# Kernel optimization log

Hardware: AMD Instinct MI355X
Metric: run time of the kernel (lower is better)

## Reference

```python
import jax, jax.numpy as jnp
import numpy as np

# dims
B, S, A = 16384, 300, 30
EMB, M_TOK, M_PROTO = 256, 8, 16
H_ENC, H_DEC, MF, NZ = 256, 128, 12, 4
ALPHA_MIN, ALPHA_MAX, ETA0 = 0.06, 0.3, 0.1
TECH_IDX = jnp.array([61, 91, 121, 151, 181, 211, 241, 271])


def setup_inputs() -> dict:
    key = jax.random.key(0)
    ks = jax.random.split(key, 20)
    def w(k, shape, fan):
        return jax.random.normal(k, shape, jnp.float32) * (fan ** -0.5)
    return {
        'state':   jax.random.uniform(ks[0], (B, S), jnp.float32),
        'fitness': jax.random.uniform(ks[1], (B, M_PROTO), jnp.float32),
        'proto_keys': jax.random.normal(ks[2], (M_PROTO, EMB), jnp.float32) * (EMB ** -0.5),
        'enc_W1': w(ks[3], (S, H_ENC), S),   'enc_b1': jnp.zeros((H_ENC,), jnp.float32),
        'ln_g':   jnp.ones((H_ENC,), jnp.float32), 'ln_b': jnp.zeros((H_ENC,), jnp.float32),
        'enc_W2': w(ks[4], (H_ENC, M_TOK * EMB), H_ENC), 'enc_b2': jnp.zeros((M_TOK * EMB,), jnp.float32),
        'dec_W1': w(ks[5], (M_PROTO, EMB, H_DEC), EMB),  'dec_b1': jnp.zeros((M_PROTO, H_DEC), jnp.float32),
        'dec_W2': w(ks[6], (M_PROTO, H_DEC, A), H_DEC),  'dec_b2': jnp.zeros((M_PROTO, A), jnp.float32),
        'tc_W':  w(ks[7], (MF, EMB), MF),  'tc_b':  jnp.zeros((EMB,), jnp.float32),
        'tc_cW': w(ks[8], (EMB, 1), EMB),  'tc_cb': jnp.zeros((1,), jnp.float32),
        'tc_zW': w(ks[9], (EMB, NZ), EMB), 'tc_zb': jnp.zeros((NZ,), jnp.float32),
        'w_prev': jnp.full((1, M_PROTO), 1.0 / M_PROTO, jnp.float32),
    }


def _layernorm(x, g, b, eps=1e-5):
    mu = x.mean(-1, keepdims=True)
    var = ((x - mu) ** 2).mean(-1, keepdims=True)
    return (x - mu) * jax.lax.rsqrt(var + eps) * g + b


def _forward(state, fitness, proto_keys, enc_W1, enc_b1, ln_g, ln_b, enc_W2, enc_b2,
             dec_W1, dec_b1, dec_W2, dec_b2, tc_W, tc_b, tc_cW, tc_cb, tc_zW, tc_zb, w_prev):
    # --- market feature extraction ---
    balance = state[:, 0:1]
    prices = state[:, 1:31]
    shares = state[:, 31:61]
    price_mean = prices.mean(1, keepdims=True)
    price_std = jnp.std(prices, axis=1, keepdims=True, ddof=1) + 1e-8  # torch.std is unbiased
    total_value = balance + (prices * shares).sum(1, keepdims=True)
    cash_ratio = balance / (total_value + 1e-8)
    tech = state[:, TECH_IDX]
    mf = jnp.concatenate([balance, price_mean, price_std, cash_ratio, tech], axis=1)  # [B,12]
    # --- T-Cell (minimal surrogate: danger embed, crisis level, crisis types) ---
    danger = jnp.tanh(mf @ tc_W + tc_b)                     # [B,EMB]
    crisis = jax.nn.sigmoid(danger @ tc_cW + tc_cb)         # [B,1]
    z = jax.nn.softmax(danger @ tc_zW + tc_zb, axis=-1)     # [B,NZ]
    # --- epitope encoder: Linear -> LN -> ReLU -> Linear -> reshape [B,m,EMB] ---
    h = jax.nn.relu(_layernorm(state @ enc_W1 + enc_b1, ln_g, ln_b))
    E = (h @ enc_W2 + enc_b2).reshape(-1, M_TOK, EMB)
    # --- IRT routing (OT-attention + fitness replicator, crisis-gated mix) ---
    scale = EMB ** -0.5
    logits = jnp.einsum('bme,ne->bmn', E, proto_keys) * scale \
           + (jnp.einsum('be,ne->bn', danger, proto_keys) * scale)[:, None, :]  # [B,m,M]
    P = jax.nn.softmax(logits, axis=-1)
    w_ot = P.mean(axis=1)                                   # [B,M]
    w_rep = w_prev * jnp.exp(ETA0 * fitness)
    w_rep = w_rep / (w_rep.sum(-1, keepdims=True) + 1e-8)
    alpha_c = ALPHA_MIN + (ALPHA_MAX - ALPHA_MIN) * (1.0 - crisis)  # [B,1]
    w = alpha_c * w_ot + (1.0 - alpha_c) * w_rep
    w = w / (w.sum(-1, keepdims=True) + 1e-8)
    # --- per-expert decoders on proto_keys (batched GEMM over M experts) ---
    hd = jax.nn.relu(jnp.einsum('me,meh->mh', proto_keys, dec_W1) + dec_b1)
    conc = jax.nn.softplus(jnp.einsum('mh,mha->ma', hd, dec_W2) + dec_b2)  # [M,A]
    mixed = jnp.einsum('bm,ma->ba', w, conc) + 1.0          # [B,A]
    # deterministic branch: softmax action head
    action = jax.nn.softmax(mixed, axis=-1)
    action = jnp.clip(action, 0.0, 1.0)
    action = action / (action.sum(-1, keepdims=True) + 1e-8)
    return action


def reference(state, fitness, proto_keys, enc_W1, enc_b1, ln_g, ln_b, enc_W2, enc_b2,
              dec_W1, dec_b1, dec_W2, dec_b2, tc_W, tc_b, tc_cW, tc_cb, tc_zW, tc_zb, w_prev):
    return _forward(state, fitness, proto_keys, enc_W1, enc_b1, ln_g, ln_b, enc_W2, enc_b2,
                    dec_W1, dec_b1, dec_W2, dec_b2, tc_W, tc_b, tc_cW, tc_cb, tc_zW, tc_zb, w_prev)
```

## Files before the change

kernel.cpp:

```cpp
#include <hip/hip_runtime.h>

typedef __attribute__((ext_vector_type(8))) short bf16x8;
typedef __attribute__((ext_vector_type(4))) float f32x4;

#define NBATCH 16384
#define SS     300
#define AA     30
#define ROWS   32
#define SSTR   352
#define HSTR   280
#define LSTR   132
#define K1P    320
#define SCALEF 0.0625f
#define ETA0   0.1f

__device__ __forceinline__ short f2b(float x) {
    unsigned u = __float_as_uint(x);
    unsigned r = (u + 0x7FFFu + ((u >> 16) & 1u)) >> 16;
    return (short)r;
}
__device__ __forceinline__ float b2f(short s) {
    return __uint_as_float(((unsigned)(unsigned short)s) << 16);
}
__device__ __forceinline__ float tanh_fast(float x) {
    float e = __expf(2.f * x);
    return 1.f - 2.f / (e + 1.f);
}

__global__ __launch_bounds__(256) void pre_kernel(
    const float* __restrict__ proto, const float* __restrict__ W2,
    const float* __restrict__ b2,   const float* __restrict__ W1,
    const float* __restrict__ dW1,  const float* __restrict__ db1,
    const float* __restrict__ dW2,  const float* __restrict__ db2,
    short* __restrict__ W1T, short* __restrict__ W3T, short* __restrict__ protoB,
    float* __restrict__ cmn, float* __restrict__ conc)
{
    const int t = threadIdx.x;
    const int bid = blockIdx.x;
    if (bid < 128) {
        const int c = bid, m = c >> 4, n = c & 15;
        __shared__ float pr[256];
        pr[t] = proto[n * 256 + t];
        __syncthreads();
        const float* w2 = W2 + (size_t)t * 2048 + m * 256;
        float acc = 0.f;
        #pragma unroll 8
        for (int e = 0; e < 256; ++e) acc += w2[e] * pr[e];
        W3T[c * 256 + t] = f2b(acc);
        if (t == 0) {
            float ca = 0.f;
            for (int e = 0; e < 256; ++e) ca += b2[m * 256 + e] * pr[e];
            cmn[c] = ca;
        }
    } else if (bid < 144) {
        const int m = bid - 128;
        __shared__ float hd[128];
        if (t < 128) {
            float acc = db1[m * 128 + t];
            const float* w = dW1 + (size_t)m * 256 * 128 + t;
            const float* p = proto + m * 256;
            for (int e = 0; e < 256; ++e) acc += p[e] * w[e * 128];
            hd[t] = fmaxf(acc, 0.f);
        }
        __syncthreads();
        if (t < AA) {
            float acc = db2[m * AA + t];
            const float* w = dW2 + (size_t)m * 128 * AA + t;
            for (int h = 0; h < 128; ++h) acc += hd[h] * w[h * AA];
            conc[m * AA + t] = fmaxf(acc, 0.f) + log1pf(__expf(-fabsf(acc)));
        }
    } else if (bid < 160) {
        const int bn = bid - 144;
        const int nl = t >> 4, kl = t & 15;
        const int n = bn * 16 + nl;
        for (int it = 0; it < 20; ++it) {
            const int k = kl + it * 16;
            const float v = (k < SS) ? W1[(size_t)k * 256 + n] : 0.f;
            W1T[n * K1P + k] = f2b(v);
        }
    } else {
        for (int i = t; i < 16 * 256; i += 256) protoB[i] = f2b(proto[i]);
    }
}

__global__ __launch_bounds__(256, 3) void main_kernel(
    const float* __restrict__ state, const float* __restrict__ fitness,
    const float* __restrict__ b1,
    const float* __restrict__ ln_g, const float* __restrict__ ln_b,
    const float* __restrict__ tcW,  const float* __restrict__ tcb,
    const float* __restrict__ cW,   const float* __restrict__ cb,
    const float* __restrict__ pw,
    const short* __restrict__ W1T,  const short* __restrict__ W3T,
    const short* __restrict__ protoB,
    const float* __restrict__ cmn,  const float* __restrict__ conc,
    float* __restrict__ out)
{
    const int t    = threadIdx.x;
    const int row0 = blockIdx.x * ROWS;
    const int w    = t >> 6;
    const int lane = t & 63;
    const int l15  = lane & 15;
    const int q    = lane >> 4;

    __shared__ short sA[ROWS * SSTR];
    __shared__ short sB[ROWS * HSTR];
    __shared__ float s_mf[ROWS][12];
    __shared__ float s_red[ROWS][8];
    __shared__ float s_mu[ROWS], s_rstd[ROWS];
    __shared__ float s_ddot[ROWS * 16];
    __shared__ float s_crisis[ROWS];
    __shared__ float s_cmn[128];
    __shared__ float s_conc[16 * AA];

    float* s_log  = (float*)sB;
    float* s_wrep = (float*)&sA[ROWS * HSTR];

    for (int idx = t; idx < ROWS * K1P; idx += 256) {
        const int r = idx / K1P, k = idx - r * K1P;
        sA[r * SSTR + k] = (k < SS) ? f2b(state[(size_t)(row0 + r) * SS + k]) : (short)0;
    }
    for (int idx = t; idx < 128 + 16 * AA; idx += 256) {
        if (idx < 128) s_cmn[idx] = cmn[idx];
        else s_conc[idx - 128] = conc[idx - 128];
    }
    __syncthreads();

    {
        const int r = t >> 3, g = t & 7;
        float sp = 0.f, sp2 = 0.f, sps = 0.f;
        const int i0 = g * 4, i1 = (g == 7) ? 2 : 4;
        for (int i = 0; i < i1; ++i) {
            const float p = b2f(sA[r * SSTR + 1 + i0 + i]);
            const float s = b2f(sA[r * SSTR + 31 + i0 + i]);
            sp += p; sp2 += p * p; sps += p * s;
        }
        for (int off = 1; off < 8; off <<= 1) {
            sp  += __shfl_xor(sp, off);
            sp2 += __shfl_xor(sp2, off);
            sps += __shfl_xor(sps, off);
        }
        s_mf[r][4 + g] = b2f(sA[r * SSTR + 61 + 30 * g]);
        if (g == 0) {
            const float bal = b2f(sA[r * SSTR + 0]);
            const float pm = sp * (1.f / 30.f);
            const float var = (sp2 - 30.f * pm * pm) * (1.f / 29.f);
            const float pstd = sqrtf(fmaxf(var, 0.f)) + 1e-8f;
            const float tv = bal + sps;
            s_mf[r][0] = bal; s_mf[r][1] = pm; s_mf[r][2] = pstd;
            s_mf[r][3] = bal / (tv + 1e-8f);
        }
    }
    __syncthreads();

    {
        float wreg[12];
        #pragma unroll
        for (int k = 0; k < 12; ++k) wreg[k] = tcW[k * 256 + t];
        const float tb = tcb[t];
        for (int r = 0; r < ROWS; ++r) {
            float acc = tb;
            #pragma unroll
            for (int k = 0; k < 12; ++k) acc = fmaf(s_mf[r][k], wreg[k], acc);
            sB[r * HSTR + t] = f2b(tanh_fast(acc));
        }
    }
    __syncthreads();

    if (w < 2) {
        f32x4 accd = {0.f, 0.f, 0.f, 0.f};
        const int mt = w;
        for (int kt = 0; kt < 8; ++kt) {
            bf16x8 a = *(const bf16x8*)&sB[(mt * 16 + l15) * HSTR + kt * 32 + q * 8];
            bf16x8 b = *(const bf16x8*)&protoB[l15 * 256 + kt * 32 + q * 8];
            accd = __builtin_amdgcn_mfma_f32_16x16x32_bf16(a, b, accd, 0, 0, 0);
        }
        #pragma unroll
        for (int reg = 0; reg < 4; ++reg) {
            const int row = mt * 16 + q * 4 + reg;
            s_ddot[row * 16 + l15] = accd[reg];
        }
    } else {
        const float4 cw = *(const float4*)&cW[lane * 4];
        const float cbv = cb[0];
        for (int rr = 0; rr < 16; ++rr) {
            const int row = (w - 2) * 16 + rr;
            const short* dp = &sB[row * HSTR + lane * 4];
            float p = b2f(dp[0]) * cw.x + b2f(dp[1]) * cw.y
                    + b2f(dp[2]) * cw.z + b2f(dp[3]) * cw.w;
            for (int off = 32; off; off >>= 1) p += __shfl_down(p, off);
            if (lane == 0) s_crisis[row] = 1.f / (1.f + __expf(-(p + cbv)));
        }
    }

    f32x4 acc[2][4];
    #pragma unroll
    for (int mt = 0; mt < 2; ++mt)
        #pragma unroll
        for (int u = 0; u < 4; ++u) acc[mt][u] = (f32x4){0.f, 0.f, 0.f, 0.f};
    for (int kt = 0; kt < 10; ++kt) {
        bf16x8 a0 = *(const bf16x8*)&sA[l15 * SSTR + kt * 32 + q * 8];
        bf16x8 a1 = *(const bf16x8*)&sA[(l15 + 16) * SSTR + kt * 32 + q * 8];
        bf16x8 bfr[4];
        #pragma unroll
        for (int u = 0; u < 4; ++u)
            bfr[u] = *(const bf16x8*)&W1T[(w * 64 + u * 16 + l15) * K1P + kt * 32 + q * 8];
        #pragma unroll
        for (int u = 0; u < 4; ++u) {
            acc[0][u] = __builtin_amdgcn_mfma_f32_16x16x32_bf16(a0, bfr[u], acc[0][u], 0, 0, 0);
            acc[1][u] = __builtin_amdgcn_mfma_f32_16x16x32_bf16(a1, bfr[u], acc[1][u], 0, 0, 0);
        }
    }

    {
        float b1v[4];
        #pragma unroll
        for (int u = 0; u < 4; ++u) b1v[u] = b1[w * 64 + u * 16 + l15];
        #pragma unroll
        for (int mt = 0; mt < 2; ++mt) {
            #pragma unroll
            for (int reg = 0; reg < 4; ++reg) {
                float s = 0.f, s2 = 0.f;
                #pragma unroll
                for (int u = 0; u < 4; ++u) {
                    const float v = acc[mt][u][reg] + b1v[u];
                    acc[mt][u][reg] = v;
                    s += v; s2 += v * v;
                }
                for (int off = 1; off < 16; off <<= 1) {
                    s  += __shfl_xor(s, off);
                    s2 += __shfl_xor(s2, off);
                }
                if (l15 == 0) {
                    const int row = mt * 16 + q * 4 + reg;
                    s_red[row][w * 2]     = s;
                    s_red[row][w * 2 + 1] = s2;
                }
            }
        }
    }
    __syncthreads();
    if (t < ROWS) {
        float S = 0.f, S2 = 0.f;
        #pragma unroll
        for (int ww = 0; ww < 4; ++ww) { S += s_red[t][2 * ww]; S2 += s_red[t][2 * ww + 1]; }
        const float mu = S * (1.f / 256.f);
        const float var = S2 * (1.f / 256.f) - mu * mu;
        s_mu[t] = mu; s_rstd[t] = rsqrtf(var + 1e-5f);
    }
    __syncthreads();

    {
        float gv[4], bv[4];
        #pragma unroll
        for (int u = 0; u < 4; ++u) {
            gv[u] = ln_g[w * 64 + u * 16 + l15];
            bv[u] = ln_b[w * 64 + u * 16 + l15];
        }
        #pragma unroll
        for (int mt = 0; mt < 2; ++mt)
            #pragma unroll
            for (int reg = 0; reg < 4; ++reg) {
                const int row = mt * 16 + q * 4 + reg;
                const float mu = s_mu[row], rs = s_rstd[row];
                #pragma unroll
                for (int u = 0; u < 4; ++u) {
                    const int col = w * 64 + u * 16 + l15;
                    const float v = fmaxf((acc[mt][u][reg] - mu) * rs * gv[u] + bv[u], 0.f);
                    sA[row * HSTR + col] = f2b(v);
                }
            }
    }
    __syncthreads();

    {
        f32x4 acc2[2][2];
        #pragma unroll
        for (int mt = 0; mt < 2; ++mt)
            #pragma unroll
            for (int ct = 0; ct < 2; ++ct) acc2[mt][ct] = (f32x4){0.f, 0.f, 0.f, 0.f};
        for (int kt = 0; kt < 8; ++kt) {
            bf16x8 a0 = *(const bf16x8*)&sA[l15 * HSTR + kt * 32 + q * 8];
            bf16x8 a1 = *(const bf16x8*)&sA[(l15 + 16) * HSTR + kt * 32 + q * 8];
            bf16x8 b0 = *(const bf16x8*)&W3T[(w * 32 + l15) * 256 + kt * 32 + q * 8];
            bf16x8 b1f = *(const bf16x8*)&W3T[(w * 32 + 16 + l15) * 256 + kt * 32 + q * 8];
            acc2[0][0] = __builtin_amdgcn_mfma_f32_16x16x32_bf16(a0, b0, acc2[0][0], 0, 0, 0);
            acc2[0][1] = __builtin_amdgcn_mfma_f32_16x16x32_bf16(a0, b1f, acc2[0][1], 0, 0, 0);
            acc2[1][0] = __builtin_amdgcn_mfma_f32_16x16x32_bf16(a1, b0, acc2[1][0], 0, 0, 0);
            acc2[1][1] = __builtin_amdgcn_mfma_f32_16x16x32_bf16(a1, b1f, acc2[1][1], 0, 0, 0);
        }
        const float cm0 = s_cmn[w * 32 + l15], cm1 = s_cmn[w * 32 + 16 + l15];
        #pragma unroll
        for (int mt = 0; mt < 2; ++mt)
            #pragma unroll
            for (int reg = 0; reg < 4; ++reg) {
                const int row = mt * 16 + q * 4 + reg;
                const float dd = s_ddot[row * 16 + l15];
                s_log[row * LSTR + w * 32 + l15]      = SCALEF * (acc2[mt][0][reg] + cm0 + dd);
                s_log[row * LSTR + w * 32 + 16 + l15] = SCALEF * (acc2[mt][1][reg] + cm1 + dd);
            }
    }
    __syncthreads();

    {
        const int r = t >> 3, m = t & 7;
        float* lg = &s_log[r * LSTR + m * 16];
        float mx = lg[0];
        #pragma unroll
        for (int n = 1; n < 16; ++n) mx = fmaxf(mx, lg[n]);
        float sum = 0.f, p[16];
        #pragma unroll
        for (int n = 0; n < 16; ++n) { p[n] = __expf(lg[n] - mx); sum += p[n]; }
        const float inv = 1.f / sum;
        #pragma unroll
        for (int n = 0; n < 16; ++n) lg[n] = p[n] * inv;
    }
    __syncthreads();

    for (int it = 0; it < 2; ++it) {
        const int idx = t + it * 256;
        const int r = idx >> 4, n = idx & 15;
        float wot = 0.f;
        #pragma unroll
        for (int m = 0; m < 8; ++m) wot += s_log[r * LSTR + m * 16 + n];
        s_ddot[idx] = wot * 0.125f;
        s_wrep[idx] = pw[n] * __expf(ETA0 * fitness[(size_t)(row0 + r) * 16 + n]);
    }
    __syncthreads();

    if (t < ROWS) {
        float srep = 0.f;
        #pragma unroll
        for (int n = 0; n < 16; ++n) srep += s_wrep[t * 16 + n];
        const float irep = 1.f / (srep + 1e-8f);
        const float alpha = 0.06f + 0.24f * (1.f - s_crisis[t]);
        float wn[16], sw = 0.f;
        #pragma unroll
        for (int n = 0; n < 16; ++n) {
            wn[n] = alpha * s_ddot[t * 16 + n] + (1.f - alpha) * s_wrep[t * 16 + n] * irep;
            sw += wn[n];
        }
        const float isw = 1.f / (sw + 1e-8f);
        #pragma unroll
        for (int n = 0; n < 16; ++n) s_ddot[t * 16 + n] = wn[n] * isw;
    }
    __syncthreads();

    {
        const int r = w * 8 + (lane >> 3);
        const int a0 = lane & 7;
        float wreg[16];
        #pragma unroll
        for (int n = 0; n < 16; ++n) wreg[n] = s_ddot[r * 16 + n];
        float mix[4];
        #pragma unroll
        for (int j = 0; j < 4; ++j) {
            const int a = a0 + 8 * j;
            if (a < AA) {
                float m = 1.f;
                #pragma unroll
                for (int n = 0; n < 16; ++n) m = fmaf(wreg[n], s_conc[n * AA + a], m);
                mix[j] = m;
            } else mix[j] = -1e30f;
        }
        float mx = fmaxf(fmaxf(mix[0], mix[1]), fmaxf(mix[2], mix[3]));
        for (int off = 1; off < 8; off <<= 1) mx = fmaxf(mx, __shfl_xor(mx, off));
        float se = 0.f;
        #pragma unroll
        for (int j = 0; j < 4; ++j) {
            if (a0 + 8 * j < AA) { mix[j] = __expf(mix[j] - mx); se += mix[j]; }
        }
        for (int off = 1; off < 8; off <<= 1) se += __shfl_xor(se, off);
        const float inv = 1.f / se;
        #pragma unroll
        for (int j = 0; j < 4; ++j) {
            const int a = a0 + 8 * j;
            if (a < AA) out[(size_t)(row0 + r) * AA + a] = mix[j] * inv;
        }
    }
}

extern "C" void kernel_launch(void* const* d_in, const int* in_sizes, int n_in,
                              void* d_out, int out_size, void* d_ws, size_t ws_size,
                              hipStream_t stream) {
    const float* state   = (const float*)d_in[0];
    const float* fitness = (const float*)d_in[1];
    const float* proto   = (const float*)d_in[2];
    const float* enc_W1  = (const float*)d_in[3];
    const float* enc_b1  = (const float*)d_in[4];
    const float* ln_g    = (const float*)d_in[5];
    const float* ln_b    = (const float*)d_in[6];
    const float* enc_W2  = (const float*)d_in[7];
    const float* enc_b2  = (const float*)d_in[8];
    const float* dec_W1  = (const float*)d_in[9];
    const float* dec_b1  = (const float*)d_in[10];
    const float* dec_W2  = (const float*)d_in[11];
    const float* dec_b2  = (const float*)d_in[12];
    const float* tc_W    = (const float*)d_in[13];
    const float* tc_b    = (const float*)d_in[14];
    const float* tc_cW   = (const float*)d_in[15];
    const float* tc_cb   = (const float*)d_in[16];
    const float* w_prev  = (const float*)d_in[19];
    float* out = (float*)d_out;

    short* W1T    = (short*)d_ws;
    short* W3T    = (short*)((char*)d_ws + 163840);
    short* protoB = (short*)((char*)d_ws + 229376);
    float* cmn    = (float*)((char*)d_ws + 237568);
    float* conc   = (float*)((char*)d_ws + 238080);

    pre_kernel<<<161, 256, 0, stream>>>(proto, enc_W2, enc_b2, enc_W1,
                                        dec_W1, dec_b1, dec_W2, dec_b2,
                                        W1T, W3T, protoB, cmn, conc);
    main_kernel<<<NBATCH / ROWS, 256, 0, stream>>>(state, fitness,
                                                   enc_b1, ln_g, ln_b,
                                                   tc_W, tc_b, tc_cW, tc_cb, w_prev,
                                                   W1T, W3T, protoB, cmn, conc, out);
}
```

Baseline: 155.0 us.

## Halve rows per block, pre-pack weights in MFMA fragment order, use MFMA for small GEMMs

Main kernel now handles 16 rows per block instead of 32, with launch bounds raised to 5 blocks per CU for higher occupancy. The pre-kernel repacks W1, W3, proto/crisis weights and tc_W into a layout that matches the MFMA B-fragment order, so each lane loads one contiguous 16-byte vector. The tech-feature projection and the crisis dot product now run as MFMA instead of scalar loops, and the W2·proto precompute also uses MFMA. The cost is that each block reuses weight loads across fewer rows, so global/L2 traffic for weights per output row goes up.

```diff
diff --git a/kernel.cpp b/kernel.cpp
--- a/kernel.cpp
+++ b/kernel.cpp
@@ -6,7 +6,7 @@
 #define NBATCH 16384
 #define SS     300
 #define AA     30
-#define ROWS   32
+#define ROWS   16
 #define SSTR   352
 #define HSTR   280
 #define LSTR   132
@@ -28,70 +28,121 @@
 }
 
 __global__ __launch_bounds__(256) void pre_kernel(
-    const float* __restrict__ proto, const float* __restrict__ W2,
-    const float* __restrict__ b2,   const float* __restrict__ W1,
+    const float* __restrict__ proto, const float* __restrict__ W1,
+    const float* __restrict__ W2,   const float* __restrict__ b2,
+    const float* __restrict__ tcW,  const float* __restrict__ cW,
     const float* __restrict__ dW1,  const float* __restrict__ db1,
     const float* __restrict__ dW2,  const float* __restrict__ db2,
-    short* __restrict__ W1T, short* __restrict__ W3T, short* __restrict__ protoB,
+    short* __restrict__ W1P, short* __restrict__ W3P,
+    short* __restrict__ PDP, short* __restrict__ TCP,
     float* __restrict__ cmn, float* __restrict__ conc)
 {
+    __shared__ short sbuf[64 * 264 + 4096];
     const int t = threadIdx.x;
     const int bid = blockIdx.x;
-    if (bid < 128) {
-        const int c = bid, m = c >> 4, n = c & 15;
-        __shared__ float pr[256];
-        pr[t] = proto[n * 256 + t];
+
+    if (bid < 32) {
+        const int m = bid >> 2, jt = bid & 3;
+        short* W2s = sbuf;
+        short* prS = sbuf + 64 * 264;
+        #pragma unroll 4
+        for (int it = 0; it < 64; ++it) {
+            const int idx = it * 256 + t, j = idx >> 8, e = idx & 255;
+            W2s[j * 264 + e] = f2b(W2[(size_t)(jt * 64 + j) * 2048 + m * 256 + e]);
+        }
+        for (int it = 0; it < 16; ++it) {
+            const int id = it * 256 + t, chunk = id >> 3, j8 = id & 7;
+            const int kt = chunk >> 6, rem = chunk & 63, q = rem >> 4, n = rem & 15;
+            prS[id] = f2b(proto[n * 256 + kt * 32 + q * 8 + j8]);
+        }
         __syncthreads();
-        const float* w2 = W2 + (size_t)t * 2048 + m * 256;
-        float acc = 0.f;
-        #pragma unroll 8
-        for (int e = 0; e < 256; ++e) acc += w2[e] * pr[e];
-        W3T[c * 256 + t] = f2b(acc);
-        if (t == 0) {
-            float ca = 0.f;
-            for (int e = 0; e < 256; ++e) ca += b2[m * 256 + e] * pr[e];
-            cmn[c] = ca;
-        }
-    } else if (bid < 144) {
-        const int m = bid - 128;
-        __shared__ float hd[128];
+        const int lane = t & 63, wv = t >> 6, l15 = lane & 15, q = lane >> 4;
+        f32x4 acc = {0.f, 0.f, 0.f, 0.f};
+        for (int kt = 0; kt < 8; ++kt) {
+            bf16x8 a = *(const bf16x8*)&W2s[(wv * 16 + l15) * 264 + kt * 32 + q * 8];
+            bf16x8 b = *(const bf16x8*)&prS[((kt * 4 + q) * 16 + l15) * 8];
+            acc = __builtin_amdgcn_mfma_f32_16x16x32_bf16(a, b, acc, 0, 0, 0);
+        }
+        #pragma unroll
+        for (int reg = 0; reg < 4; ++reg) {
+            const int jg = jt * 64 + wv * 16 + q * 4 + reg;
+            const int c = m * 16 + l15;
+            const int ktj = jg >> 5, qj = (jg >> 3) & 3, j8 = jg & 7;
+            W3P[((ktj * 4 + qj) * 128 + c) * 8 + j8] = f2b(acc[reg]);
+        }
+    } else if (bid < 42) {
+        const int kt = bid - 32;
+        short* W1s = sbuf;
+        #pragma unroll 4
+        for (int it = 0; it < 32; ++it) {
+            const int idx = it * 256 + t, k = idx >> 8, n = idx & 255;
+            const int kg = kt * 32 + k;
+            W1s[k * 256 + n] = (kg < SS) ? f2b(W1[(size_t)kg * 256 + n]) : (short)0;
+        }
+        __syncthreads();
+        for (int it = 0; it < 4; ++it) {
+            const int id = it * 256 + t, q = id >> 8, n = id & 255;
+            bf16x8 v;
+            #pragma unroll
+            for (int j = 0; j < 8; ++j) v[j] = W1s[(q * 8 + j) * 256 + n];
+            *(bf16x8*)&W1P[((kt * 4 + q) * 256 + n) * 8] = v;
+        }
+    } else if (bid == 42) {
+        for (int it = 0; it < 32; ++it) {
+            const int id = it * 256 + t, chunk = id >> 3, j8 = id & 7;
+            const int kt = chunk >> 7, q = (chunk >> 5) & 3, np = chunk & 31;
+            const int k = kt * 32 + q * 8 + j8;
+            float v = 0.f;
+            if (np < 16) v = proto[np * 256 + k];
+            else if (np == 16) v = cW[k];
+            PDP[id] = f2b(v);
+        }
+    } else if (bid == 43) {
+        for (int it = 0; it < 32; ++it) {
+            const int id = it * 256 + t, chunk = id >> 3, j8 = id & 7;
+            const int q = chunk >> 8, n = chunk & 255, k = q * 8 + j8;
+            TCP[id] = (k < 12) ? f2b(tcW[k * 256 + n]) : (short)0;
+        }
+    } else if (bid == 44) {
+        float* b2s = (float*)sbuf;
+        float* prF = (float*)sbuf + 2048;
+        for (int it = 0; it < 8; ++it)  b2s[it * 256 + t] = b2[it * 256 + t];
+        for (int it = 0; it < 16; ++it) prF[it * 256 + t] = proto[it * 256 + t];
+        __syncthreads();
+        if (t < 128) {
+            const int mq = t >> 4, n = t & 15;
+            float acc = 0.f;
+            for (int e = 0; e < 256; ++e) acc += b2s[mq * 256 + e] * prF[n * 256 + e];
+            cmn[t] = acc;
+        }
+    } else {
+        const int m = bid - 45;
+        float* hd = (float*)sbuf;
         if (t < 128) {
             float acc = db1[m * 128 + t];
-            const float* w = dW1 + (size_t)m * 256 * 128 + t;
+            const float* wp = dW1 + (size_t)m * 256 * 128 + t;
             const float* p = proto + m * 256;
-            for (int e = 0; e < 256; ++e) acc += p[e] * w[e * 128];
+            for (int e = 0; e < 256; ++e) acc += p[e] * wp[e * 128];
             hd[t] = fmaxf(acc, 0.f);
         }
         __syncthreads();
         if (t < AA) {
             float acc = db2[m * AA + t];
-            const float* w = dW2 + (size_t)m * 128 * AA + t;
-            for (int h = 0; h < 128; ++h) acc += hd[h] * w[h * AA];
+            const float* wp = dW2 + (size_t)m * 128 * AA + t;
+            for (int h = 0; h < 128; ++h) acc += hd[h] * wp[h * AA];
             conc[m * AA + t] = fmaxf(acc, 0.f) + log1pf(__expf(-fabsf(acc)));
         }
-    } else if (bid < 160) {
-        const int bn = bid - 144;
-        const int nl = t >> 4, kl = t & 15;
-        const int n = bn * 16 + nl;
-        for (int it = 0; it < 20; ++it) {
-            const int k = kl + it * 16;
-            const float v = (k < SS) ? W1[(size_t)k * 256 + n] : 0.f;
-            W1T[n * K1P + k] = f2b(v);
-        }
-    } else {
-        for (int i = t; i < 16 * 256; i += 256) protoB[i] = f2b(proto[i]);
-    }
-}
-
-__global__ __launch_bounds__(256, 3) void main_kernel(
+    }
+}
+
+__global__ __launch_bounds__(256, 5) void main_kernel(
     const float* __restrict__ state, const float* __restrict__ fitness,
     const float* __restrict__ b1,
-    const float* __restrict__ ln_g, const float* __restrict__ ln_b,
-    const float* __restrict__ tcW,  const float* __restrict__ tcb,
-    const float* __restrict__ cW,   const float* __restrict__ cb,
+    const float* __restrict__ lng,  const float* __restrict__ lnb,
+    const float* __restrict__ tcb,  const float* __restrict__ cb,
     const float* __restrict__ pw,
-    const short* __restrict__ W1T,  const short* __restrict__ W3T,
-    const short* __restrict__ protoB,
+    const short* __restrict__ W1P,  const short* __restrict__ W3P,
+    const short* __restrict__ PDP,  const short* __restrict__ TCP,
     const float* __restrict__ cmn,  const float* __restrict__ conc,
     float* __restrict__ out)
 {
@@ -104,10 +155,10 @@
 
     __shared__ short sA[ROWS * SSTR];
     __shared__ short sB[ROWS * HSTR];
-    __shared__ float s_mf[ROWS][12];
+    __shared__ short s_mfB[ROWS * 32];
     __shared__ float s_red[ROWS][8];
     __shared__ float s_mu[ROWS], s_rstd[ROWS];
-    __shared__ float s_ddot[ROWS * 16];
+    __shared__ float s_dd[ROWS * 16];
     __shared__ float s_crisis[ROWS];
     __shared__ float s_cmn[128];
     __shared__ float s_conc[16 * AA];
@@ -115,126 +166,132 @@
     float* s_log  = (float*)sB;
     float* s_wrep = (float*)&sA[ROWS * HSTR];
 
-    for (int idx = t; idx < ROWS * K1P; idx += 256) {
-        const int r = idx / K1P, k = idx - r * K1P;
+    #pragma unroll 4
+    for (int it = 0; it < 20; ++it) {
+        const int idx = it * 256 + t, r = idx / K1P, k = idx - r * K1P;
         sA[r * SSTR + k] = (k < SS) ? f2b(state[(size_t)(row0 + r) * SS + k]) : (short)0;
     }
-    for (int idx = t; idx < 128 + 16 * AA; idx += 256) {
-        if (idx < 128) s_cmn[idx] = cmn[idx];
-        else s_conc[idx - 128] = conc[idx - 128];
-    }
-    __syncthreads();
-
-    {
-        const int r = t >> 3, g = t & 7;
+    for (int it = t; it < 128 + 16 * AA; it += 256) {
+        if (it < 128) s_cmn[it] = cmn[it];
+        else s_conc[it - 128] = conc[it - 128];
+    }
+    __syncthreads();
+
+    {
+        const int r = t >> 4, g = t & 15;
         float sp = 0.f, sp2 = 0.f, sps = 0.f;
-        const int i0 = g * 4, i1 = (g == 7) ? 2 : 4;
-        for (int i = 0; i < i1; ++i) {
-            const float p = b2f(sA[r * SSTR + 1 + i0 + i]);
-            const float s = b2f(sA[r * SSTR + 31 + i0 + i]);
-            sp += p; sp2 += p * p; sps += p * s;
-        }
-        for (int off = 1; off < 8; off <<= 1) {
+        if (g < 15) {
+            #pragma unroll
+            for (int jj = 0; jj < 2; ++jj) {
+                const int i = 2 * g + jj;
+                const float p = b2f(sA[r * SSTR + 1 + i]);
+                const float s = b2f(sA[r * SSTR + 31 + i]);
+                sp += p; sp2 += p * p; sps += p * s;
+            }
+        }
+        #pragma unroll
+        for (int off = 1; off < 16; off <<= 1) {
             sp  += __shfl_xor(sp, off);
             sp2 += __shfl_xor(sp2, off);
             sps += __shfl_xor(sps, off);
         }
-        s_mf[r][4 + g] = b2f(sA[r * SSTR + 61 + 30 * g]);
+        if (g < 8) s_mfB[r * 32 + 4 + g] = sA[r * SSTR + 61 + 30 * g];
+        for (int k = 12 + g; k < 32; k += 16) s_mfB[r * 32 + k] = 0;
         if (g == 0) {
-            const float bal = b2f(sA[r * SSTR + 0]);
+            const float bal = b2f(sA[r * SSTR]);
             const float pm = sp * (1.f / 30.f);
             const float var = (sp2 - 30.f * pm * pm) * (1.f / 29.f);
             const float pstd = sqrtf(fmaxf(var, 0.f)) + 1e-8f;
-            const float tv = bal + sps;
-            s_mf[r][0] = bal; s_mf[r][1] = pm; s_mf[r][2] = pstd;
-            s_mf[r][3] = bal / (tv + 1e-8f);
-        }
-    }
-    __syncthreads();
-
-    {
-        float wreg[12];
-        #pragma unroll
-        for (int k = 0; k < 12; ++k) wreg[k] = tcW[k * 256 + t];
-        const float tb = tcb[t];
-        for (int r = 0; r < ROWS; ++r) {
-            float acc = tb;
-            #pragma unroll
-            for (int k = 0; k < 12; ++k) acc = fmaf(s_mf[r][k], wreg[k], acc);
-            sB[r * HSTR + t] = f2b(tanh_fast(acc));
-        }
-    }
-    __syncthreads();
-
-    if (w < 2) {
-        f32x4 accd = {0.f, 0.f, 0.f, 0.f};
-        const int mt = w;
+            s_mfB[r * 32 + 0] = sA[r * SSTR];
+            s_mfB[r * 32 + 1] = f2b(pm);
+            s_mfB[r * 32 + 2] = f2b(pstd);
+            s_mfB[r * 32 + 3] = f2b(bal / (bal + sps + 1e-8f));
+        }
+    }
+    __syncthreads();
+
+    {
+        f32x4 dacc[4];
+        #pragma unroll
+        for (int u = 0; u < 4; ++u) dacc[u] = (f32x4){0.f, 0.f, 0.f, 0.f};
+        bf16x8 a = *(const bf16x8*)&s_mfB[l15 * 32 + q * 8];
+        #pragma unroll
+        for (int u = 0; u < 4; ++u) {
+            bf16x8 b = *(const bf16x8*)&TCP[((q << 8) | (w * 64 + u * 16 + l15)) * 8];
+            dacc[u] = __builtin_amdgcn_mfma_f32_16x16x32_bf16(a, b, dacc[u], 0, 0, 0);
+        }
+        #pragma unroll
+        for (int u = 0; u < 4; ++u) {
+            const int col = w * 64 + u * 16 + l15;
+            const float tb = tcb[col];
+            #pragma unroll
+            for (int reg = 0; reg < 4; ++reg)
+                sB[(q * 4 + reg) * HSTR + col] = f2b(tanh_fast(dacc[u][reg] + tb));
+        }
+    }
+    __syncthreads();
+
+    if (w == 0) {
+        f32x4 acc = {0.f, 0.f, 0.f, 0.f};
         for (int kt = 0; kt < 8; ++kt) {
-            bf16x8 a = *(const bf16x8*)&sB[(mt * 16 + l15) * HSTR + kt * 32 + q * 8];
-            bf16x8 b = *(const bf16x8*)&protoB[l15 * 256 + kt * 32 + q * 8];
-            accd = __builtin_amdgcn_mfma_f32_16x16x32_bf16(a, b, accd, 0, 0, 0);
-        }
+            bf16x8 a = *(const bf16x8*)&sB[l15 * HSTR + kt * 32 + q * 8];
+            bf16x8 b = *(const bf16x8*)&PDP[((kt * 4 + q) * 32 + l15) * 8];
+            acc = __builtin_amdgcn_mfma_f32_16x16x32_bf16(a, b, acc, 0, 0, 0);
+        }
+        #pragma unroll
+        for (int reg = 0; reg < 4; ++reg)
+            s_dd[(q * 4 + reg) * 16 + l15] = acc[reg];
+    } else if (w == 1) {
+        f32x4 acc = {0.f, 0.f, 0.f, 0.f};
+        for (int kt = 0; kt < 8; ++kt) {
+            bf16x8 a = *(const bf16x8*)&sB[l15 * HSTR + kt * 32 + q * 8];
+            bf16x8 b = *(const bf16x8*)&PDP[((kt * 4 + q) * 32 + 16 + l15) * 8];
+            acc = __builtin_amdgcn_mfma_f32_16x16x32_bf16(a, b, acc, 0, 0, 0);
+        }
+        if (l15 == 0) {
+            const float cbv = cb[0];
+            #pragma unroll
+            for (int reg = 0; reg < 4; ++reg)
+                s_crisis[q * 4 + reg] = 1.f / (1.f + __expf(-(acc[reg] + cbv)));
+        }
+    }
+
+    f32x4 acc[4];
+    #pragma unroll
+    for (int u = 0; u < 4; ++u) acc[u] = (f32x4){0.f, 0.f, 0.f, 0.f};
+    for (int kt = 0; kt < 10; ++kt) {
+        bf16x8 a = *(const bf16x8*)&sA[l15 * SSTR + kt * 32 + q * 8];
+        bf16x8 bfr[4];
+        #pragma unroll
+        for (int u = 0; u < 4; ++u)
+            bfr[u] = *(const bf16x8*)&W1P[((kt * 4 + q) * 256 + (w * 64 + u * 16 + l15)) * 8];
+        #pragma unroll
+        for (int u = 0; u < 4; ++u)
+            acc[u] = __builtin_amdgcn_mfma_f32_16x16x32_bf16(a, bfr[u], acc[u], 0, 0, 0);
+    }
+
+    {
+        float b1v[4];
+        #pragma unroll
+        for (int u = 0; u < 4; ++u) b1v[u] = b1[w * 64 + u * 16 + l15];
         #pragma unroll
         for (int reg = 0; reg < 4; ++reg) {
-            const int row = mt * 16 + q * 4 + reg;
-            s_ddot[row * 16 + l15] = accd[reg];
-        }
-    } else {
-        const float4 cw = *(const float4*)&cW[lane * 4];
-        const float cbv = cb[0];
-        for (int rr = 0; rr < 16; ++rr) {
-            const int row = (w - 2) * 16 + rr;
-            const short* dp = &sB[row * HSTR + lane * 4];
-            float p = b2f(dp[0]) * cw.x + b2f(dp[1]) * cw.y
-                    + b2f(dp[2]) * cw.z + b2f(dp[3]) * cw.w;
-            for (int off = 32; off; off >>= 1) p += __shfl_down(p, off);
-            if (lane == 0) s_crisis[row] = 1.f / (1.f + __expf(-(p + cbv)));
-        }
-    }
-
-    f32x4 acc[2][4];
-    #pragma unroll
-    for (int mt = 0; mt < 2; ++mt)
-        #pragma unroll
-        for (int u = 0; u < 4; ++u) acc[mt][u] = (f32x4){0.f, 0.f, 0.f, 0.f};
-    for (int kt = 0; kt < 10; ++kt) {
-        bf16x8 a0 = *(const bf16x8*)&sA[l15 * SSTR + kt * 32 + q * 8];
-        bf16x8 a1 = *(const bf16x8*)&sA[(l15 + 16) * SSTR + kt * 32 + q * 8];
-        bf16x8 bfr[4];
-        #pragma unroll
-        for (int u = 0; u < 4; ++u)
-            bfr[u] = *(const bf16x8*)&W1T[(w * 64 + u * 16 + l15) * K1P + kt * 32 + q * 8];
-        #pragma unroll
-        for (int u = 0; u < 4; ++u) {
-            acc[0][u] = __builtin_amdgcn_mfma_f32_16x16x32_bf16(a0, bfr[u], acc[0][u], 0, 0, 0);
-            acc[1][u] = __builtin_amdgcn_mfma_f32_16x16x32_bf16(a1, bfr[u], acc[1][u], 0, 0, 0);
-        }
-    }
-
-    {
-        float b1v[4];
-        #pragma unroll
-        for (int u = 0; u < 4; ++u) b1v[u] = b1[w * 64 + u * 16 + l15];
-        #pragma unroll
-        for (int mt = 0; mt < 2; ++mt) {
-            #pragma unroll
-            for (int reg = 0; reg < 4; ++reg) {
-                float s = 0.f, s2 = 0.f;
-                #pragma unroll
-                for (int u = 0; u < 4; ++u) {
-                    const float v = acc[mt][u][reg] + b1v[u];
-                    acc[mt][u][reg] = v;
-                    s += v; s2 += v * v;
-                }
-                for (int off = 1; off < 16; off <<= 1) {
-                    s  += __shfl_xor(s, off);
-                    s2 += __shfl_xor(s2, off);
-                }
-                if (l15 == 0) {
-                    const int row = mt * 16 + q * 4 + reg;
-                    s_red[row][w * 2]     = s;
-                    s_red[row][w * 2 + 1] = s2;
-                }
+            float s = 0.f, s2 = 0.f;
+            #pragma unroll
+            for (int u = 0; u < 4; ++u) {
+                const float v = acc[u][reg] + b1v[u];
+                acc[u][reg] = v;
+                s += v; s2 += v * v;
+            }
+            #pragma unroll
+            for (int off = 1; off < 16; off <<= 1) {
+                s  += __shfl_xor(s, off);
+                s2 += __shfl_xor(s2, off);
+            }
+            if (l15 == 0) {
+                const int row = q * 4 + reg;
+                s_red[row][w * 2]     = s;
+                s_red[row][w * 2 + 1] = s2;
             }
         }
     }
@@ -253,55 +310,46 @@
         float gv[4], bv[4];
         #pragma unroll
         for (int u = 0; u < 4; ++u) {
-            gv[u] = ln_g[w * 64 + u * 16 + l15];
-            bv[u] = ln_b[w * 64 + u * 16 + l15];
-        }
-        #pragma unroll
-        for (int mt = 0; mt < 2; ++mt)
-            #pragma unroll
-            for (int reg = 0; reg < 4; ++reg) {
-                const int row = mt * 16 + q * 4 + reg;
-                const float mu = s_mu[row], rs = s_rstd[row];
-                #pragma unroll
-                for (int u = 0; u < 4; ++u) {
-                    const int col = w * 64 + u * 16 + l15;
-                    const float v = fmaxf((acc[mt][u][reg] - mu) * rs * gv[u] + bv[u], 0.f);
-                    sA[row * HSTR + col] = f2b(v);
-                }
+            gv[u] = lng[w * 64 + u * 16 + l15];
+            bv[u] = lnb[w * 64 + u * 16 + l15];
+        }
+        #pragma unroll
+        for (int reg = 0; reg < 4; ++reg) {
+            const int row = q * 4 + reg;
+            const float mu = s_mu[row], rs = s_rstd[row];
+            #pragma unroll
+            for (int u = 0; u < 4; ++u) {
+                const int col = w * 64 + u * 16 + l15;
+                const float v = fmaxf((acc[u][reg] - mu) * rs * gv[u] + bv[u], 0.f);
+                sA[row * HSTR + col] = f2b(v);
             }
-    }
-    __syncthreads();
-
-    {
-        f32x4 acc2[2][2];
-        #pragma unroll
-        for (int mt = 0; mt < 2; ++mt)
-            #pragma unroll
-            for (int ct = 0; ct < 2; ++ct) acc2[mt][ct] = (f32x4){0.f, 0.f, 0.f, 0.f};
+        }
+    }
+    __syncthreads();
+
+    {
+        f32x4 c2[2];
+        c2[0] = (f32x4){0.f, 0.f, 0.f, 0.f};
+        c2[1] = (f32x4){0.f, 0.f, 0.f, 0.f};
         for (int kt = 0; kt < 8; ++kt) {
-            bf16x8 a0 = *(const bf16x8*)&sA[l15 * HSTR + kt * 32 + q * 8];
-            bf16x8 a1 = *(const bf16x8*)&sA[(l15 + 16) * HSTR + kt * 32 + q * 8];
-            bf16x8 b0 = *(const bf16x8*)&W3T[(w * 32 + l15) * 256 + kt * 32 + q * 8];
-            bf16x8 b1f = *(const bf16x8*)&W3T[(w * 32 + 16 + l15) * 256 + kt * 32 + q * 8];
-            acc2[0][0] = __builtin_amdgcn_mfma_f32_16x16x32_bf16(a0, b0, acc2[0][0], 0, 0, 0);
-            acc2[0][1] = __builtin_amdgcn_mfma_f32_16x16x32_bf16(a0, b1f, acc2[0][1], 0, 0, 0);
-            acc2[1][0] = __builtin_amdgcn_mfma_f32_16x16x32_bf16(a1, b0, acc2[1][0], 0, 0, 0);
-            acc2[1][1] = __builtin_amdgcn_mfma_f32_16x16x32_bf16(a1, b1f, acc2[1][1], 0, 0, 0);
+            bf16x8 a = *(const bf16x8*)&sA[l15 * HSTR + kt * 32 + q * 8];
+            bf16x8 b0 = *(const bf16x8*)&W3P[((kt * 4 + q) * 128 + w * 32 + l15) * 8];
+            bf16x8 b1f = *(const bf16x8*)&W3P[((kt * 4 + q) * 128 + w * 32 + 16 + l15) * 8];
+            c2[0] = __builtin_amdgcn_mfma_f32_16x16x32_bf16(a, b0, c2[0], 0, 0, 0);
+            c2[1] = __builtin_amdgcn_mfma_f32_16x16x32_bf16(a, b1f, c2[1], 0, 0, 0);
         }
         const float cm0 = s_cmn[w * 32 + l15], cm1 = s_cmn[w * 32 + 16 + l15];
         #pragma unroll
-        for (int mt = 0; mt < 2; ++mt)
-            #pragma unroll
-            for (int reg = 0; reg < 4; ++reg) {
-                const int row = mt * 16 + q * 4 + reg;
-                const float dd = s_ddot[row * 16 + l15];
-                s_log[row * LSTR + w * 32 + l15]      = SCALEF * (acc2[mt][0][reg] + cm0 + dd);
-                s_log[row * LSTR + w * 32 + 16 + l15] = SCALEF * (acc2[mt][1][reg] + cm1 + dd);
-            }
-    }
-    __syncthreads();
-
-    {
+        for (int reg = 0; reg < 4; ++reg) {
+            const int row = q * 4 + reg;
+            const float dd = s_dd[row * 16 + l15];
+            s_log[row * LSTR + w * 32 + l15]      = SCALEF * (c2[0][reg] + cm0 + dd);
+            s_log[row * LSTR + w * 32 + 16 + l15] = SCALEF * (c2[1][reg] + cm1 + dd);
+        }
+    }
+    __syncthreads();
+
+    if (t < 128) {
         const int r = t >> 3, m = t & 7;
         float* lg = &s_log[r * LSTR + m * 16];
         float mx = lg[0];
@@ -316,14 +364,13 @@
     }
     __syncthreads();
 
-    for (int it = 0; it < 2; ++it) {
-        const int idx = t + it * 256;
-        const int r = idx >> 4, n = idx & 15;
+    {
+        const int r = t >> 4, n = t & 15;
         float wot = 0.f;
         #pragma unroll
         for (int m = 0; m < 8; ++m) wot += s_log[r * LSTR + m * 16 + n];
-        s_ddot[idx] = wot * 0.125f;
-        s_wrep[idx] = pw[n] * __expf(ETA0 * fitness[(size_t)(row0 + r) * 16 + n]);
+        s_dd[t] = wot * 0.125f;
+        s_wrep[t] = pw[n] * __expf(ETA0 * fitness[(size_t)(row0 + r) * 16 + n]);
     }
     __syncthreads();
 
@@ -336,46 +383,41 @@
         float wn[16], sw = 0.f;
         #pragma unroll
         for (int n = 0; n < 16; ++n) {
-            wn[n] = alpha * s_ddot[t * 16 + n] + (1.f - alpha) * s_wrep[t * 16 + n] * irep;
+            wn[n] = alpha * s_dd[t * 16 + n] + (1.f - alpha) * s_wrep[t * 16 + n] * irep;
             sw += wn[n];
         }
         const float isw = 1.f / (sw + 1e-8f);
         #pragma unroll
-        for (int n = 0; n < 16; ++n) s_ddot[t * 16 + n] = wn[n] * isw;
-    }
-    __syncthreads();
-
-    {
-        const int r = w * 8 + (lane >> 3);
-        const int a0 = lane & 7;
+        for (int n = 0; n < 16; ++n) s_dd[t * 16 + n] = wn[n] * isw;
+    }
+    __syncthreads();
+
+    {
+        const int r = w * 4 + q;
+        const int a0 = l15;
+        const int a1 = a0 + 16;
+        const bool v1 = a1 < AA;
         float wreg[16];
         #pragma unroll
-        for (int n = 0; n < 16; ++n) wreg[n] = s_ddot[r * 16 + n];
-        float mix[4];
-        #pragma unroll
-        for (int j = 0; j < 4; ++j) {
-            const int a = a0 + 8 * j;
-            if (a < AA) {
-                float m = 1.f;
-                #pragma unroll
-                for (int n = 0; n < 16; ++n) m = fmaf(wreg[n], s_conc[n * AA + a], m);
-                mix[j] = m;
-            } else mix[j] = -1e30f;
-        }
-        float mx = fmaxf(fmaxf(mix[0], mix[1]), fmaxf(mix[2], mix[3]));
-        for (int off = 1; off < 8; off <<= 1) mx = fmaxf(mx, __shfl_xor(mx, off));
-        float se = 0.f;
-        #pragma unroll
-        for (int j = 0; j < 4; ++j) {
-            if (a0 + 8 * j < AA) { mix[j] = __expf(mix[j] - mx); se += mix[j]; }
-        }
-        for (int off = 1; off < 8; off <<= 1) se += __shfl_xor(se, off);
+        for (int n = 0; n < 16; ++n) wreg[n] = s_dd[r * 16 + n];
+        float m0 = 1.f, m1 = 1.f;
+        const int a1s = v1 ? a1 : 0;
+        #pragma unroll
+        for (int n = 0; n < 16; ++n) {
+            m0 = fmaf(wreg[n], s_conc[n * AA + a0], m0);
+            m1 = fmaf(wreg[n], s_conc[n * AA + a1s], m1);
+        }
+        float mx = v1 ? fmaxf(m0, m1) : m0;
+        #pragma unroll
+        for (int off = 1; off < 16; off <<= 1) mx = fmaxf(mx, __shfl_xor(mx, off));
+        float e0 = __expf(m0 - mx);
+        float e1 = v1 ? __expf(m1 - mx) : 0.f;
+        float se = e0 + e1;
+        #pragma unroll
+        for (int off = 1; off < 16; off <<= 1) se += __shfl_xor(se, off);
         const float inv = 1.f / se;
-        #pragma unroll
-        for (int j = 0; j < 4; ++j) {
-            const int a = a0 + 8 * j;
-            if (a < AA) out[(size_t)(row0 + r) * AA + a] = mix[j] * inv;
-        }
+        out[(size_t)(row0 + r) * AA + a0] = e0 * inv;
+        if (v1) out[(size_t)(row0 + r) * AA + a1] = e1 * inv;
     }
 }
 
@@ -402,17 +444,19 @@
     const float* w_prev  = (const float*)d_in[19];
     float* out = (float*)d_out;
 
-    short* W1T    = (short*)d_ws;
-    short* W3T    = (short*)((char*)d_ws + 163840);
-    short* protoB = (short*)((char*)d_ws + 229376);
-    float* cmn    = (float*)((char*)d_ws + 237568);
-    float* conc   = (float*)((char*)d_ws + 238080);
-
-    pre_kernel<<<161, 256, 0, stream>>>(proto, enc_W2, enc_b2, enc_W1,
-                                        dec_W1, dec_b1, dec_W2, dec_b2,
-                                        W1T, W3T, protoB, cmn, conc);
+    short* W1P = (short*)d_ws;
+    short* W3P = W1P + 81920;
+    short* PDP = W3P + 32768;
+    short* TCP = PDP + 8192;
+    float* cmn  = (float*)(TCP + 8192);
+    float* conc = cmn + 128;
+
+    pre_kernel<<<61, 256, 0, stream>>>(proto, enc_W1, enc_W2, enc_b2,
+                                       tc_W, tc_cW,
+                                       dec_W1, dec_b1, dec_W2, dec_b2,
+                                       W1P, W3P, PDP, TCP, cmn, conc);
     main_kernel<<<NBATCH / ROWS, 256, 0, stream>>>(state, fitness,
                                                    enc_b1, ln_g, ln_b,
-                                                   tc_W, tc_b, tc_cW, tc_cb, w_prev,
-                                                   W1T, W3T, protoB, cmn, conc, out);
-}
+                                                   tc_b, tc_cb, w_prev,
+                                                   W1P, W3P, PDP, TCP, cmn, conc, out);
+}
```

Measured after the change: 133.6 us. 1.16x faster.
